# Performance work log

Hardware: AMD Instinct MI355X
Metric: run time of the kernel (lower is better)

Reference implementation:

```python
import jax, jax.numpy as jnp
import numpy as np

EMBED = 512
HEADS = 8
HEAD_DIM = EMBED // HEADS


def setup_inputs() -> dict:
    key = jax.random.key(0)
    ks = jax.random.split(key, 9)
    B, P, S, E = 32, 512, 1024, EMBED
    query = jax.random.normal(ks[0], (B, P, E), dtype=jnp.float32)
    k_in = jax.random.normal(ks[1], (B, S, E), dtype=jnp.float32)
    v_in = jax.random.normal(ks[2], (B, S, E), dtype=jnp.float32)
    key_padding_mask = jax.random.randint(ks[3], (B, P, S), 0, 2).astype(bool)
    sc = 1.0 / np.sqrt(E)
    Wq = jax.random.normal(ks[4], (E, E), dtype=jnp.float32) * sc
    Wk = jax.random.normal(ks[5], (E, E), dtype=jnp.float32) * sc
    Wv = jax.random.normal(ks[6], (E, E), dtype=jnp.float32) * sc
    Wo = jax.random.normal(ks[7], (E, E), dtype=jnp.float32) * sc
    bo = jax.random.normal(ks[8], (E,), dtype=jnp.float32) * 0.01
    return {"query": query, "key": k_in, "value": v_in,
            "key_padding_mask": key_padding_mask,
            "Wq": Wq, "Wk": Wk, "Wv": Wv, "Wo": Wo, "bo": bo}


def reference(query, key, value, key_padding_mask, Wq, Wk, Wv, Wo, bo):
    B, P, E = query.shape
    S = key.shape[1]
    H, D = HEADS, HEAD_DIM
    scale = D ** -0.5
    # Linear projections (torch Linear: x @ W.T)
    Q = (query @ Wq.T).reshape(B, P, H, D).transpose(0, 2, 1, 3)  # [B,H,P,D]
    K = (key @ Wk.T).reshape(B, S, H, D).transpose(0, 2, 1, 3)    # [B,H,S,D]
    V = (value @ Wv.T).reshape(B, S, H, D).transpose(0, 2, 1, 3)  # [B,H,S,D]
    scores = jnp.einsum('bhpd,bhsd->bhps', Q, K) * scale          # [B,H,P,S]
    mask = key_padding_mask[:, None, :, :]                        # [B,1,P,S]
    scores = jnp.where(mask, -jnp.inf, scores)
    attn = jax.nn.softmax(scores, axis=-1)
    ctx = jnp.einsum('bhps,bhsd->bhpd', attn, V)                  # [B,H,P,D]
    ctx = ctx.transpose(0, 2, 1, 3).reshape(B, P, E)
    return ctx @ Wo.T + bo
```

## Files before the change

kernel.cpp:

```cpp
#include <hip/hip_runtime.h>

#define B_  32
#define P_  512
#define S_  1024
#define E_  512
#define H_  8
#define D_  64

typedef unsigned int uint32;
typedef unsigned short u16;
typedef __attribute__((ext_vector_type(8))) _Float16 half8;
typedef __attribute__((ext_vector_type(2))) __fp16 fp16x2;
typedef __attribute__((ext_vector_type(4))) float f32x4;
typedef __attribute__((ext_vector_type(2))) uint32 u32x2;

__device__ __forceinline__ u16 f2h_bits(float f){
  _Float16 h = (_Float16)f;
  union { _Float16 h; u16 u; } cv; cv.h = h; return cv.u;
}
__device__ __forceinline__ uint32 pk16(float a, float b){
  union { fp16x2 h; uint32 u; } cv;
  cv.h = __builtin_amdgcn_cvt_pkrtz(a, b);
  return cv.u;
}
__device__ __forceinline__ half8 cvt8(f32x4 a, f32x4 b){
  half8 h;
  h[0]=(_Float16)a[0]; h[1]=(_Float16)a[1]; h[2]=(_Float16)a[2]; h[3]=(_Float16)a[3];
  h[4]=(_Float16)b[0]; h[5]=(_Float16)b[1]; h[6]=(_Float16)b[2]; h[7]=(_Float16)b[3];
  return h;
}
__device__ __forceinline__ f32x4 mfma16(half8 a, half8 b, f32x4 c){
  return __builtin_amdgcn_mfma_f32_16x16x32_f16(a, b, c, 0, 0, 0);
}
__device__ __forceinline__ int swz(int row, int col){ return row*64 + (col ^ ((row & 7) << 3)); }
#define GLD16(ldsp, gp) __builtin_amdgcn_global_load_lds( \
    (const __attribute__((address_space(1))) void*)(gp), \
    (__attribute__((address_space(3))) void*)(ldsp), 16, 0, 0)

__global__ void cvt_w_kernel(const float* __restrict__ w0, const float* __restrict__ w1,
                             const float* __restrict__ w2, const float* __restrict__ w3,
                             u16* __restrict__ out){
  int i = blockIdx.x * 256 + threadIdx.x;
  int region = i >> 15;
  int off = (i & 32767) * 8;
  const float* s = (region == 0) ? w0 : (region == 1) ? w1 : (region == 2) ? w2 : w3;
  f32x4 a = *(const f32x4*)(s + off);
  f32x4 b = *(const f32x4*)(s + off + 4);
  int row = off >> 9;
  int k   = off & 511;
  int ks  = (region < 3) ? ((k & ~63) | ((k & 63) ^ ((row & 7) << 3))) : k;
  *(half8*)(out + region * 262144 + row*512 + ks) = cvt8(a, b);
}

__global__ void detect_mask_kernel(const uint32* __restrict__ m, int* __restrict__ flag){
  __shared__ int s_gt1, s_bgt1;
  if (threadIdx.x == 0){ s_gt1 = 0; s_bgt1 = 0; }
  __syncthreads();
  int gt1 = 0, bgt1 = 0;
  for (int i = threadIdx.x; i < 4096; i += 256){
    uint32 w = m[i];
    if (w > 1u) gt1 = 1;
    if (((w)&0xffu) > 1u || ((w>>8)&0xffu) > 1u || ((w>>16)&0xffu) > 1u || ((w>>24)&0xffu) > 1u) bgt1 = 1;
  }
  if (gt1)  atomicOr(&s_gt1, 1);
  if (bgt1) atomicOr(&s_bgt1, 1);
  __syncthreads();
  if (threadIdx.x == 0) *flag = s_gt1 ? (s_bgt1 ? 2 : 1) : 0;
}

__global__ void pack_mask_kernel(const uint32* __restrict__ m, const int* __restrict__ flag,
                                 uint32* __restrict__ bits){
  const int w = blockIdx.x * 256 + threadIdx.x;
  const int f = *flag;
  uint32 out = 0u;
  if (f == 1){
    #pragma unroll
    for (int i = 0; i < 8; i++){
      uint32 v = m[(size_t)w*8 + i];
      if (v & 0x000000ffu) out |= 1u << (i*4 + 0);
      if (v & 0x0000ff00u) out |= 1u << (i*4 + 1);
      if (v & 0x00ff0000u) out |= 1u << (i*4 + 2);
      if (v & 0xff000000u) out |= 1u << (i*4 + 3);
    }
  } else {
    #pragma unroll
    for (int i = 0; i < 32; i++){
      if (m[(size_t)w*32 + i]) out |= 1u << i;
    }
  }
  bits[w] = out;
}

template<int MODE>
__global__ __launch_bounds__(256) void gemm_proj(
    const u16* __restrict__ Wsz, const float* __restrict__ Act,
    u16* __restrict__ Cp, int rshift, float scale)
{
  __shared__ __align__(16) u16 As[128*64];
  __shared__ __align__(16) u16 Bs[128*64];
  const int tid  = threadIdx.x;
  const int lane = tid & 63;
  const int wv   = tid >> 6;
  const int lrow = lane & 15, khi = lane >> 4;
  const int wm   = wv >> 1,  wn  = wv & 1;

  const int nwg = gridDim.x;
  const int bid = blockIdx.x;
  const int l   = (bid & 7) * (nwg >> 3) + (bid >> 3);
  const int by  = l & 3;
  const long bxL = l >> 2;

  const long gm0 = (long)by * 128;
  const long gn0 = bxL * 128;
  const int  srow = tid >> 1, scb = (tid & 1) * 32;

  f32x4 acc[4][4];
  #pragma unroll
  for (int i = 0; i < 4; i++)
    #pragma unroll
    for (int j = 0; j < 4; j++) acc[i][j] = (f32x4){0.f,0.f,0.f,0.f};

  #pragma unroll 1
  for (int kk = 0; kk < 512; kk += 64){
    if (kk) __syncthreads();
    #pragma unroll
    for (int j = 0; j < 4; j++){
      int row = j*32 + (tid >> 3);
      GLD16(&As[j*2048 + tid*8], Wsz + (gm0 + row)*512 + kk + (tid & 7)*8);
    }
    {
      const float* bp = Act + (gn0 + srow)*512 + kk + scb;
      #pragma unroll
      for (int i = 0; i < 4; i++){
        f32x4 f0 = *(const f32x4*)(bp + i*8);
        f32x4 f1 = *(const f32x4*)(bp + i*8 + 4);
        *(half8*)&Bs[swz(srow, scb + i*8)] = cvt8(f0, f1);
      }
    }
    __syncthreads();

    half8 af[4][2], bf[4][2];
    #pragma unroll
    for (int mi = 0; mi < 4; mi++){
      const int r_ = wm*64 + mi*16 + lrow;
      af[mi][0] = *(const half8*)&As[swz(r_, khi*8)];
      af[mi][1] = *(const half8*)&As[swz(r_, khi*8 + 32)];
    }
    #pragma unroll
    for (int ni = 0; ni < 4; ni++){
      const int r_ = wn*64 + ni*16 + lrow;
      bf[ni][0] = *(const half8*)&Bs[swz(r_, khi*8)];
      bf[ni][1] = *(const half8*)&Bs[swz(r_, khi*8 + 32)];
    }
    #pragma unroll
    for (int mi = 0; mi < 4; mi++)
      #pragma unroll
      for (int ni = 0; ni < 4; ni++){
        acc[mi][ni] = mfma16(af[mi][0], bf[ni][0], acc[mi][ni]);
        acc[mi][ni] = mfma16(af[mi][1], bf[ni][1], acc[mi][ni]);
      }
  }

  #pragma unroll
  for (int mi = 0; mi < 4; mi++)
    #pragma unroll
    for (int ni = 0; ni < 4; ni++){
      f32x4 v = acc[mi][ni];
      const long arow = gn0 + wn*64 + ni*16 + lrow;
      if (MODE == 0){
        const int h  = (int)(gm0 >> 6) + wm;
        const int d0 = mi*16 + khi*4;
        const long b  = arow >> rshift;
        const long rr = arow & ((1L << rshift) - 1);
        u32x2 p;
        p.x = pk16(v[0]*scale, v[1]*scale);
        p.y = pk16(v[2]*scale, v[3]*scale);
        *(u32x2*)&Cp[(((b*8 + h) << rshift) + rr)*64 + d0] = p;
      } else {
        const long n = gm0 + wm*64 + mi*16 + khi*4;
        const long b = arow >> 10, s = arow & 1023;
        #pragma unroll
        for (int r = 0; r < 4; r++)
          Cp[b*524288 + (n + r)*1024 + s] = f2h_bits(v[r]);
      }
    }
}

__global__ __launch_bounds__(256) void gemm_out(
    const u16* __restrict__ Ap, const u16* __restrict__ Bp,
    float* __restrict__ Cp, const float* __restrict__ bias)
{
  __shared__ __align__(16) u16 As[128*64];
  __shared__ __align__(16) u16 Bs[128*64];
  const int tid  = threadIdx.x;
  const int lane = tid & 63;
  const int wv   = tid >> 6;
  const int lrow = lane & 15, khi = lane >> 4;
  const int wm   = wv >> 1,  wn  = wv & 1;

  int bx = blockIdx.x, by = blockIdx.y;
  {
    const int nbx = gridDim.x;
    const int nwg = nbx * gridDim.y;
    const int bid = by * nbx + bx;
    const int l = (bid & 7) * (nwg >> 3) + (bid >> 3);
    by = l / nbx; bx = l - by * nbx;
  }
  const long gm0 = (long)by * 128;
  const long gn0 = (long)bx * 128;

  f32x4 acc[4][4];
  #pragma unroll
  for (int i = 0; i < 4; i++)
    #pragma unroll
    for (int j = 0; j < 4; j++) acc[i][j] = (f32x4){0.f,0.f,0.f,0.f};

  #pragma unroll 1
  for (int kk = 0; kk < 512; kk += 64){
    if (kk) __syncthreads();
    #pragma unroll
    for (int j = 0; j < 4; j++){
      int row = j*32 + (tid >> 3);
      GLD16(&As[j*2048 + tid*8], Ap + (gm0 + row)*512 + kk + (tid & 7)*8);
      GLD16(&Bs[j*2048 + tid*8], Bp + (gn0 + row)*512 + kk + (tid & 7)*8);
    }
    __syncthreads();

    half8 af[4][2], bf[4][2];
    #pragma unroll
    for (int mi = 0; mi < 4; mi++){
      const u16* p = &As[(wm*64 + mi*16 + lrow)*64 + khi*8];
      af[mi][0] = *(const half8*)p;
      af[mi][1] = *(const half8*)(p + 32);
    }
    #pragma unroll
    for (int ni = 0; ni < 4; ni++){
      const u16* p = &Bs[(wn*64 + ni*16 + lrow)*64 + khi*8];
      bf[ni][0] = *(const half8*)p;
      bf[ni][1] = *(const half8*)(p + 32);
    }
    #pragma unroll
    for (int mi = 0; mi < 4; mi++)
      #pragma unroll
      for (int ni = 0; ni < 4; ni++){
        acc[mi][ni] = mfma16(af[mi][0], bf[ni][0], acc[mi][ni]);
        acc[mi][ni] = mfma16(af[mi][1], bf[ni][1], acc[mi][ni]);
      }
  }

  #pragma unroll
  for (int mi = 0; mi < 4; mi++)
    #pragma unroll
    for (int ni = 0; ni < 4; ni++)
      #pragma unroll
      for (int r = 0; r < 4; r++){
        long gm = gm0 + wm*64 + mi*16 + khi*4 + r;
        long gn = gn0 + wn*64 + ni*16 + lrow;
        Cp[gm*512 + gn] = acc[mi][ni][r] + bias[gn];
      }
}

__global__ __launch_bounds__(256) void attn_kernel(
    const u16* __restrict__ Qb, const u16* __restrict__ Kb,
    const u16* __restrict__ Vtb, const uint32* __restrict__ bits,
    u16* __restrict__ Ctx)
{
  __shared__ __align__(16) u16 Ks[64*64];
  __shared__ __align__(16) u16 Vs[64*64];

  const int tid  = threadIdx.x;
  const int lane = tid & 63;
  const int wv   = tid >> 6;
  const int lrow = lane & 15, khi = lane >> 4;

  const int bidx = blockIdx.x;
  const int logical = (bidx & 7) * 256 + (bidx >> 3);
  const int bh = logical >> 3;
  const int p0 = (logical & 7) * 64;
  const int bb = bh >> 3;

  const u16* qp = Qb  + (size_t)bh * (P_*64) + (size_t)p0 * 64;
  const u16* kp = Kb  + (size_t)bh * (S_*64);
  const u16* vp = Vtb + (size_t)bh * (D_*S_);
  const int srow = tid >> 2, scb = (tid & 3) * 16;
  const size_t mbase = (size_t)(bb*P_ + p0 + wv*16 + lrow) * (S_/32);

  half8 kr0 = *(const half8*)(kp + (size_t)srow*64 + scb);
  half8 kr1 = *(const half8*)(kp + (size_t)srow*64 + scb + 8);
  half8 vr0 = *(const half8*)(vp + (size_t)srow*S_ + scb);
  half8 vr1 = *(const half8*)(vp + (size_t)srow*S_ + scb + 8);
  uint32 mw0 = bits[mbase], mw1 = bits[mbase + 1];

  {
    const u16* src = qp + (size_t)srow*64 + scb;
    *(half8*)&Ks[swz(srow, scb)]     = *(const half8*)src;
    *(half8*)&Ks[swz(srow, scb + 8)] = *(const half8*)(src + 8);
  }
  __syncthreads();
  half8 q_lo = *(const half8*)&Ks[swz(wv*16 + lrow, khi*8)];
  half8 q_hi = *(const half8*)&Ks[swz(wv*16 + lrow, khi*8 + 32)];

  f32x4 accO[4];
  #pragma unroll
  for (int i = 0; i < 4; i++) accO[i] = (f32x4){0.f,0.f,0.f,0.f};
  float mst = -1e30f, lst = 0.f;

  const int srcA = (lrow + 16*((2*khi)    & 3)) << 2;
  const int srcB = (lrow + 16*((2*khi + 1)& 3)) << 2;
  const bool hiH = khi >= 2;

  #pragma unroll 1
  for (int t = 0; t < 16; t++){
    __syncthreads();
    *(half8*)&Ks[swz(srow, scb)]     = kr0;
    *(half8*)&Ks[swz(srow, scb + 8)] = kr1;
    *(half8*)&Vs[swz(srow, scb)]     = vr0;
    *(half8*)&Vs[swz(srow, scb + 8)] = vr1;
    __syncthreads();
    const uint32 cm0 = mw0, cm1 = mw1;
    if (t < 15){
      const u16* kn = kp + (size_t)(t + 1)*4096 + (size_t)srow*64 + scb;
      kr0 = *(const half8*)kn; kr1 = *(const half8*)(kn + 8);
      const u16* vn = vp + (size_t)srow*S_ + (t + 1)*64 + scb;
      vr0 = *(const half8*)vn; vr1 = *(const half8*)(vn + 8);
      mw0 = bits[mbase + (t + 1)*2]; mw1 = bits[mbase + (t + 1)*2 + 1];
    }

    f32x4 sc[4];
    __builtin_amdgcn_s_setprio(1);
    #pragma unroll
    for (int ssub = 0; ssub < 4; ssub++){
      const int rr = ssub*16 + lrow;
      half8 k_lo = *(const half8*)&Ks[swz(rr, khi*8)];
      half8 k_hi = *(const half8*)&Ks[swz(rr, khi*8 + 32)];
      f32x4 c = (f32x4){0.f,0.f,0.f,0.f};
      c = mfma16(k_lo, q_lo, c);
      c = mfma16(k_hi, q_hi, c);
      sc[ssub] = c;
    }
    __builtin_amdgcn_s_setprio(0);

    float mx = -1e30f;
    #pragma unroll
    for (int ssub = 0; ssub < 4; ssub++){
      const uint32 mw = (ssub < 2) ? cm0 : cm1;
      #pragma unroll
      for (int r = 0; r < 4; r++){
        const int s = ssub*16 + khi*4 + r;
        float v = sc[ssub][r];
        if ((mw >> (s & 31)) & 1u) v = -1e30f;
        sc[ssub][r] = v;
        mx = fmaxf(mx, v);
      }
    }
    mx = fmaxf(mx, __shfl_xor(mx, 16));
    mx = fmaxf(mx, __shfl_xor(mx, 32));
    if (__any(mx - mst > 8.f)){
      const float mnew = fmaxf(mst, mx);
      const float fac = __builtin_amdgcn_exp2f(mst - mnew);
      lst *= fac;
      #pragma unroll
      for (int d = 0; d < 4; d++){
        f32x4 a = accO[d];
        a[0] *= fac; a[1] *= fac; a[2] *= fac; a[3] *= fac;
        accO[d] = a;
      }
      mst = mnew;
    }
    float ts = 0.f;
    #pragma unroll
    for (int ssub = 0; ssub < 4; ssub++)
      #pragma unroll
      for (int r = 0; r < 4; r++){
        float p = __builtin_amdgcn_exp2f(sc[ssub][r] - mst);
        sc[ssub][r] = p;
        ts += p;
      }
    ts += __shfl_xor(ts, 16);
    ts += __shfl_xor(ts, 32);
    lst += ts;

    uint32 w00 = pk16(sc[0][0], sc[0][1]), w01 = pk16(sc[0][2], sc[0][3]);
    uint32 w10 = pk16(sc[1][0], sc[1][1]), w11 = pk16(sc[1][2], sc[1][3]);
    uint32 w20 = pk16(sc[2][0], sc[2][1]), w21 = pk16(sc[2][2], sc[2][3]);
    uint32 w30 = pk16(sc[3][0], sc[3][1]), w31 = pk16(sc[3][2], sc[3][3]);

    union { half8 h; uint32 u[4]; } plo, phi;
    {
      uint32 t0, t1;
      t0 = __builtin_amdgcn_ds_bpermute(srcA, (int)w00);
      t1 = __builtin_amdgcn_ds_bpermute(srcA, (int)w10);
      plo.u[0] = hiH ? t1 : t0;
      t0 = __builtin_amdgcn_ds_bpermute(srcA, (int)w01);
      t1 = __builtin_amdgcn_ds_bpermute(srcA, (int)w11);
      plo.u[1] = hiH ? t1 : t0;
      t0 = __builtin_amdgcn_ds_bpermute(srcB, (int)w00);
      t1 = __builtin_amdgcn_ds_bpermute(srcB, (int)w10);
      plo.u[2] = hiH ? t1 : t0;
      t0 = __builtin_amdgcn_ds_bpermute(srcB, (int)w01);
      t1 = __builtin_amdgcn_ds_bpermute(srcB, (int)w11);
      plo.u[3] = hiH ? t1 : t0;
      t0 = __builtin_amdgcn_ds_bpermute(srcA, (int)w20);
      t1 = __builtin_amdgcn_ds_bpermute(srcA, (int)w30);
      phi.u[0] = hiH ? t1 : t0;
      t0 = __builtin_amdgcn_ds_bpermute(srcA, (int)w21);
      t1 = __builtin_amdgcn_ds_bpermute(srcA, (int)w31);
      phi.u[1] = hiH ? t1 : t0;
      t0 = __builtin_amdgcn_ds_bpermute(srcB, (int)w20);
      t1 = __builtin_amdgcn_ds_bpermute(srcB, (int)w30);
      phi.u[2] = hiH ? t1 : t0;
      t0 = __builtin_amdgcn_ds_bpermute(srcB, (int)w21);
      t1 = __builtin_amdgcn_ds_bpermute(srcB, (int)w31);
      phi.u[3] = hiH ? t1 : t0;
    }

    __builtin_amdgcn_s_setprio(1);
    #pragma unroll
    for (int dsub = 0; dsub < 4; dsub++){
      const int rr = dsub*16 + lrow;
      half8 v_lo = *(const half8*)&Vs[swz(rr, khi*8)];
      half8 v_hi = *(const half8*)&Vs[swz(rr, khi*8 + 32)];
      accO[dsub] = mfma16(v_lo, plo.h, accO[dsub]);
      accO[dsub] = mfma16(v_hi, phi.h, accO[dsub]);
    }
    __builtin_amdgcn_s_setprio(0);
  }

  const int hh = bh & 7;
  const float inv = __builtin_amdgcn_rcpf(lst);
  const size_t base = (size_t)(bb*P_ + p0 + wv*16 + lrow) * E_ + hh*64 + khi*4;
  #pragma unroll
  for (int dsub = 0; dsub < 4; dsub++){
    u32x2 pkd;
    pkd.x = pk16(accO[dsub][0] * inv, accO[dsub][1] * inv);
    pkd.y = pk16(accO[dsub][2] * inv, accO[dsub][3] * inv);
    *(u32x2*)&Ctx[base + dsub*16] = pkd;
  }
}

extern "C" void kernel_launch(void* const* d_in, const int* in_sizes, int n_in,
                              void* d_out, int out_size, void* d_ws, size_t ws_size,
                              hipStream_t stream)
{
  const float* query = (const float*)d_in[0];
  const float* key   = (const float*)d_in[1];
  const float* value = (const float*)d_in[2];
  const void*  mask  = d_in[3];
  const float* Wq = (const float*)d_in[4];
  const float* Wk = (const float*)d_in[5];
  const float* Wv = (const float*)d_in[6];
  const float* Wo = (const float*)d_in[7];
  const float* bo = (const float*)d_in[8];

  char* ws = (char*)d_ws;
  u16*    Qb   = (u16*)(ws);
  u16*    Kb   = (u16*)(ws + (16u << 20));
  u16*    Vtb  = (u16*)(ws + (48u << 20));
  u16*    Ctx  = (u16*)(ws + (80u << 20));
  u16*    W4h  = (u16*)(ws + (96u << 20));
  uint32* bits = (uint32*)d_out;
  int*    flag = (int*)((char*)d_out + (2u << 20));

  const float SCLQ = 0.125f * 1.44269504f;

  cvt_w_kernel<<<512, 256, 0, stream>>>(Wq, Wk, Wv, Wo, W4h);
  detect_mask_kernel<<<1, 256, 0, stream>>>((const uint32*)mask, flag);
  pack_mask_kernel<<<2048, 256, 0, stream>>>((const uint32*)mask, flag, bits);
  gemm_proj<0><<<512, 256, 0, stream>>>(W4h, query, Qb, 9, SCLQ);
  gemm_proj<0><<<1024, 256, 0, stream>>>(W4h + 262144, key, Kb, 10, 1.0f);
  gemm_proj<1><<<1024, 256, 0, stream>>>(W4h + 524288, value, Vtb, 0, 1.0f);
  attn_kernel<<<2048, 256, 0, stream>>>(Qb, Kb, Vtb, bits, Ctx);
  gemm_out<<<dim3(4, 128), 256, 0, stream>>>(Ctx, W4h + 786432, (float*)d_out, bo);
}
```

Measured before the change: 426.3 us.

## Double-buffer weight tiles and prefetch activations in projection GEMM; vectorize mask packing

The projection GEMM now double-buffers the weight tile in shared memory and prefetches the next activation slice into registers while the current tile's MFMAs run. The converted half-precision activations are written to shared memory after a barrier, and the MFMA block is wrapped in raised wave priority. The mask packing kernel also switches to 16-byte vector loads. The aim is to hide global load latency behind compute, at the cost of extra shared memory and register pressure that may lower occupancy.

```diff
diff --git a/kernel.cpp b/kernel.cpp
--- a/kernel.cpp
+++ b/kernel.cpp
@@ -13,6 +13,7 @@
 typedef __attribute__((ext_vector_type(2))) __fp16 fp16x2;
 typedef __attribute__((ext_vector_type(4))) float f32x4;
 typedef __attribute__((ext_vector_type(2))) uint32 u32x2;
+typedef __attribute__((ext_vector_type(4))) uint32 u32x4;
 
 __device__ __forceinline__ u16 f2h_bits(float f){
   _Float16 h = (_Float16)f;
@@ -75,17 +76,25 @@
   uint32 out = 0u;
   if (f == 1){
     #pragma unroll
+    for (int i = 0; i < 2; i++){
+      u32x4 v = *(const u32x4*)(m + (size_t)w*8 + i*4);
+      #pragma unroll
+      for (int j = 0; j < 4; j++){
+        uint32 x = v[j];
+        if (x & 0x000000ffu) out |= 1u << (i*16 + j*4 + 0);
+        if (x & 0x0000ff00u) out |= 1u << (i*16 + j*4 + 1);
+        if (x & 0x00ff0000u) out |= 1u << (i*16 + j*4 + 2);
+        if (x & 0xff000000u) out |= 1u << (i*16 + j*4 + 3);
+      }
+    }
+  } else {
+    #pragma unroll
     for (int i = 0; i < 8; i++){
-      uint32 v = m[(size_t)w*8 + i];
-      if (v & 0x000000ffu) out |= 1u << (i*4 + 0);
-      if (v & 0x0000ff00u) out |= 1u << (i*4 + 1);
-      if (v & 0x00ff0000u) out |= 1u << (i*4 + 2);
-      if (v & 0xff000000u) out |= 1u << (i*4 + 3);
-    }
-  } else {
-    #pragma unroll
-    for (int i = 0; i < 32; i++){
-      if (m[(size_t)w*32 + i]) out |= 1u << i;
+      u32x4 v = *(const u32x4*)(m + (size_t)w*32 + i*4);
+      if (v[0]) out |= 1u << (i*4 + 0);
+      if (v[1]) out |= 1u << (i*4 + 1);
+      if (v[2]) out |= 1u << (i*4 + 2);
+      if (v[3]) out |= 1u << (i*4 + 3);
     }
   }
   bits[w] = out;
@@ -96,7 +105,7 @@
     const u16* __restrict__ Wsz, const float* __restrict__ Act,
     u16* __restrict__ Cp, int rshift, float scale)
 {
-  __shared__ __align__(16) u16 As[128*64];
+  __shared__ __align__(16) u16 As[2][128*64];
   __shared__ __align__(16) u16 Bs[128*64];
   const int tid  = threadIdx.x;
   const int lane = tid & 63;
@@ -113,6 +122,20 @@
   const long gm0 = (long)by * 128;
   const long gn0 = bxL * 128;
   const int  srow = tid >> 1, scb = (tid & 1) * 32;
+  const float* bp0 = Act + (gn0 + srow)*512 + scb;
+
+  f32x4 breg[8];
+  #pragma unroll
+  for (int j = 0; j < 4; j++){
+    int row = j*32 + (tid >> 3);
+    GLD16(&As[0][j*2048 + tid*8], Wsz + (gm0 + row)*512 + (tid & 7)*8);
+  }
+  #pragma unroll
+  for (int i = 0; i < 8; i++) breg[i] = *(const f32x4*)(bp0 + i*4);
+  #pragma unroll
+  for (int i = 0; i < 4; i++)
+    *(half8*)&Bs[swz(srow, scb + i*8)] = cvt8(breg[2*i], breg[2*i+1]);
+  __syncthreads();
 
   f32x4 acc[4][4];
   #pragma unroll
@@ -121,30 +144,26 @@
     for (int j = 0; j < 4; j++) acc[i][j] = (f32x4){0.f,0.f,0.f,0.f};
 
   #pragma unroll 1
-  for (int kk = 0; kk < 512; kk += 64){
-    if (kk) __syncthreads();
-    #pragma unroll
-    for (int j = 0; j < 4; j++){
-      int row = j*32 + (tid >> 3);
-      GLD16(&As[j*2048 + tid*8], Wsz + (gm0 + row)*512 + kk + (tid & 7)*8);
-    }
-    {
-      const float* bp = Act + (gn0 + srow)*512 + kk + scb;
-      #pragma unroll
-      for (int i = 0; i < 4; i++){
-        f32x4 f0 = *(const f32x4*)(bp + i*8);
-        f32x4 f1 = *(const f32x4*)(bp + i*8 + 4);
-        *(half8*)&Bs[swz(srow, scb + i*8)] = cvt8(f0, f1);
-      }
-    }
-    __syncthreads();
+  for (int t = 0; t < 8; t++){
+    const int kk = t * 64;
+    const u16* Acur = &As[t & 1][0];
+    if (t < 7){
+      u16* Anx = &As[(t + 1) & 1][0];
+      #pragma unroll
+      for (int j = 0; j < 4; j++){
+        int row = j*32 + (tid >> 3);
+        GLD16(&Anx[j*2048 + tid*8], Wsz + (gm0 + row)*512 + kk + 64 + (tid & 7)*8);
+      }
+      #pragma unroll
+      for (int i = 0; i < 8; i++) breg[i] = *(const f32x4*)(bp0 + kk + 64 + i*4);
+    }
 
     half8 af[4][2], bf[4][2];
     #pragma unroll
     for (int mi = 0; mi < 4; mi++){
       const int r_ = wm*64 + mi*16 + lrow;
-      af[mi][0] = *(const half8*)&As[swz(r_, khi*8)];
-      af[mi][1] = *(const half8*)&As[swz(r_, khi*8 + 32)];
+      af[mi][0] = *(const half8*)&Acur[swz(r_, khi*8)];
+      af[mi][1] = *(const half8*)&Acur[swz(r_, khi*8 + 32)];
     }
     #pragma unroll
     for (int ni = 0; ni < 4; ni++){
@@ -152,6 +171,7 @@
       bf[ni][0] = *(const half8*)&Bs[swz(r_, khi*8)];
       bf[ni][1] = *(const half8*)&Bs[swz(r_, khi*8 + 32)];
     }
+    __builtin_amdgcn_s_setprio(1);
     #pragma unroll
     for (int mi = 0; mi < 4; mi++)
       #pragma unroll
@@ -159,6 +179,14 @@
         acc[mi][ni] = mfma16(af[mi][0], bf[ni][0], acc[mi][ni]);
         acc[mi][ni] = mfma16(af[mi][1], bf[ni][1], acc[mi][ni]);
       }
+    __builtin_amdgcn_s_setprio(0);
+    __syncthreads();
+    if (t < 7){
+      #pragma unroll
+      for (int i = 0; i < 4; i++)
+        *(half8*)&Bs[swz(srow, scb + i*8)] = cvt8(breg[2*i], breg[2*i+1]);
+      __syncthreads();
+    }
   }
 
   #pragma unroll
```

Result: slower. 441.3 us (+3.5%).
